# Optimization experiments

Hardware: AMD Instinct MI355X
Metric: run time of the kernel (lower is better)

Reference implementation:

```python
import jax, jax.numpy as jnp
import numpy as np

N_RAYS = 8192
N_SAMPLES = 128
HIDDEN = 128
SH_DIM = 16
RAY_EXT_FACTOR = 10.0


def rsh_cart_3(d):
    # Real spherical harmonics up to degree 3, Cartesian form (16 coeffs).
    x, y, z = d[..., 0], d[..., 1], d[..., 2]
    x2, y2, z2 = x * x, y * y, z * z
    xy, yz, xz = x * y, y * z, x * z
    return jnp.stack([
        0.282094791773878 * jnp.ones_like(x),
        -0.48860251190292 * y,
        0.48860251190292 * z,
        -0.48860251190292 * x,
        1.0925484305920792 * xy,
        -1.0925484305920792 * yz,
        0.94617469575756 * z2 - 0.31539156525252,
        -1.0925484305920792 * xz,
        0.5462742152960396 * (x2 - y2),
        0.5900435899266435 * y * (-3.0 * x2 + y2),
        2.8906114426405538 * xy * z,
        0.4570457994644658 * y * (1.0 - 5.0 * z2),
        0.3731763325901154 * z * (5.0 * z2 - 3.0),
        0.4570457994644658 * x * (1.0 - 5.0 * z2),
        1.445305721320277 * z * (x2 - y2),
        0.5900435899266435 * x * (-x2 + 3.0 * y2),
    ], axis=-1)


def setup_inputs() -> dict:
    key = jax.random.key(0)
    ks = jax.random.split(key, 11)
    o = jax.random.normal(ks[0], (N_RAYS, 3), dtype=jnp.float32)
    origins = 2.5 * o / jnp.linalg.norm(o, axis=-1, keepdims=True)
    # aim roughly at the unit AABB so most rays are active
    dirs = -origins + 0.2 * jax.random.normal(ks[1], (N_RAYS, 3), dtype=jnp.float32)
    u = jax.random.uniform(ks[2], (N_RAYS, N_SAMPLES), dtype=jnp.float32)
    s1 = 1.0 / np.sqrt(3.0)
    s2 = 1.0 / np.sqrt(HIDDEN)
    s3 = 1.0 / np.sqrt(HIDDEN + SH_DIM)
    return {
        'origins': origins,
        'dirs': dirs,
        'u': u,
        'W1': s1 * jax.random.normal(ks[3], (3, HIDDEN), dtype=jnp.float32),
        'b1': jnp.zeros((HIDDEN,), jnp.float32),
        'W2': s2 * jax.random.normal(ks[4], (HIDDEN, HIDDEN), dtype=jnp.float32),
        'b2': jnp.zeros((HIDDEN,), jnp.float32),
        'Wd': s2 * jax.random.normal(ks[5], (HIDDEN, 1), dtype=jnp.float32),
        'bd': jnp.zeros((1,), jnp.float32),
        'Wc': s3 * jax.random.normal(ks[6], (HIDDEN + SH_DIM, 3), dtype=jnp.float32),
        'bc': jnp.zeros((3,), jnp.float32),
    }


def reference(origins, dirs, u, W1, b1, W2, b2, Wd, bd, Wc, bc):
    B, T = u.shape
    # ---- AABB ([-1,1]^3) slab intersection -> tnear/tfar, active mask ----
    inv_d = 1.0 / dirs
    t1 = (-1.0 - origins) * inv_d
    t2 = (1.0 - origins) * inv_d
    tnear = jnp.maximum(jnp.max(jnp.minimum(t1, t2), axis=-1), 0.0)  # (B,)
    tfar = jnp.min(jnp.maximum(t1, t2), axis=-1)                      # (B,)
    active = tfar > tnear                                             # (B,)
    tfar_c = jnp.maximum(tfar, tnear + 1e-3)
    # ---- stratified ray step sampling ----
    frac = (jnp.arange(T, dtype=u.dtype) + u) / T                     # (B,T)
    ts = tnear[:, None] + (tfar_c - tnear)[:, None] * frac            # (B,T)
    xyz = origins[:, None, :] + dirs[:, None, :] * ts[..., None]      # (B,T,3)
    # aabb is [-1,1]^3 so ndc == xyz; spatial filter = bounds test
    xyz_ndc = xyz
    mask = jnp.all(jnp.abs(xyz_ndc) <= 1.0, axis=-1) & active[:, None]  # (B,T)
    dnorm = jnp.linalg.norm(dirs, axis=-1)                            # (B,)
    ynm = rsh_cart_3(dirs / dnorm[:, None])                           # (B,16)
    # ---- radiance field MLP over all sample points ----
    x = xyz_ndc.reshape(B * T, 3)
    h = jax.nn.relu(x @ W1 + b1)
    h = jax.nn.relu(h @ W2 + b2)
    sigma = jax.nn.softplus(h @ Wd + bd).reshape(B, T)
    cond = jnp.broadcast_to(ynm[:, None, :], (B, T, SH_DIM)).reshape(B * T, SH_DIM)
    color = jax.nn.sigmoid(jnp.concatenate([h, cond], axis=-1) @ Wc + bc).reshape(B, T, 3)
    # zero out points rejected by the spatial filter (torch writes only masked)
    sigma = sigma * mask
    color = color * mask[..., None]
    # ---- transmittance integration (integrate_timesteps) ----
    tfinal = tfar_c * RAY_EXT_FACTOR
    deltas = jnp.diff(ts, axis=-1, append=tfinal[:, None])            # (B,T)
    sd = sigma * deltas * dnorm[:, None]
    csum = jnp.cumsum(sd, axis=-1)
    # weights_i = T_i * alpha_i = exp(-csum_{i-1}) - exp(-csum_i)
    weights = jnp.exp(sd - csum) - jnp.exp(-csum)                     # (B,T)
    color_out = jnp.einsum('bt,btc->bc', weights, color)              # (B,3)
    alpha_out = jnp.sum(weights, axis=-1, keepdims=True)              # (B,1)
    rgba = jnp.concatenate([color_out, alpha_out], axis=-1)           # (B,4)
    return jnp.where(active[:, None], rgba, 0.0)
```

## Files before the change

kernel.cpp:

```cpp
#include <hip/hip_runtime.h>
#include <math.h>

#define NRAYS 8192
#define T 128
#define H 128
#define SHD 16

using short8 = __attribute__((ext_vector_type(8))) short;
using f32x4  = __attribute__((ext_vector_type(4))) float;

__device__ __forceinline__ float softplus_f(float x) {
  return fmaxf(x, 0.f) + log1pf(expf(-fabsf(x)));
}

__device__ __forceinline__ unsigned f2bf(float f) {
  unsigned u = __float_as_uint(f);
  return (u + 0x7fffu + ((u >> 16) & 1u)) >> 16;
}

__device__ __forceinline__ unsigned pkbf(float a, float b) {
  const unsigned ua = __float_as_uint(a) + 0x8000u;
  const unsigned ub = __float_as_uint(b) + 0x8000u;
  return __builtin_amdgcn_perm(ub, ua, 0x07060302u);
}

__global__ void preprocess(const float* __restrict__ W2, const float* __restrict__ Wd,
                           const float* __restrict__ Wc,
                           unsigned short* __restrict__ w2t,
                           unsigned short* __restrict__ woutf) {
  const int t = blockIdx.x * 256 + threadIdx.x;
  if (t < 16384) {
    const int n = t >> 7, p = t & 127;
    const int o = (p >> 3) ^ (n & 7);
    const int k = o * 8 + (p & 7);
    w2t[t] = (unsigned short)f2bf(W2[k * 128 + n]);
  }
  if (t < 2048) {
    const int kk = t >> 9, L = (t >> 3) & 63, j = t & 7;
    const int c = L & 15, g = L >> 4;
    const int k = kk * 32 + g * 8 + j;
    float v = 0.f;
    if (c == 0) v = Wd[k];
    else if (c < 4) v = Wc[k * 3 + (c - 1)];
    woutf[t] = (unsigned short)f2bf(v);
  }
}

__global__ __launch_bounds__(256, 3) void nerf_render(
    const float* __restrict__ origins, const float* __restrict__ dirs,
    const float* __restrict__ u, const float* __restrict__ W1,
    const float* __restrict__ b1, const float* __restrict__ b2,
    const float* __restrict__ bd, const float* __restrict__ Wc,
    const float* __restrict__ bc, const unsigned short* __restrict__ w2t,
    const unsigned short* __restrict__ woutf, float* __restrict__ out)
{
  const int ray = blockIdx.x;
  const int tid = threadIdx.x;
  const int L = tid & 63;
  const int w = tid >> 6;
  const int g = L >> 4;
  const int c = L & 15;

  __shared__ __align__(16) short Bs[16384];
  __shared__ __align__(16) short As2[4 * 640];
  __shared__ __align__(16) float2 bsl[H];
  __shared__ float ts_s[T];
  __shared__ float mask_s[T];
  __shared__ __align__(16) float4 SredP[T];
  __shared__ float rayp[8];
  __shared__ float wred[2][4];
  __shared__ float wtot[2];

  {
    const float4* src = (const float4*)w2t;
    float4* dst = (float4*)Bs;
    #pragma unroll
    for (int i = 0; i < 8; ++i) dst[tid + i * 256] = src[tid + i * 256];
  }

  if (tid < T) {
    const int tl = tid;
    const float ox = origins[ray*3+0], oy = origins[ray*3+1], oz = origins[ray*3+2];
    const float dx = dirs[ray*3+0],  dy = dirs[ray*3+1],  dz = dirs[ray*3+2];
    const float ix = 1.f/dx, iy = 1.f/dy, iz = 1.f/dz;
    const float t1x = (-1.f-ox)*ix, t2x = (1.f-ox)*ix;
    const float t1y = (-1.f-oy)*iy, t2y = (1.f-oy)*iy;
    const float t1z = (-1.f-oz)*iz, t2z = (1.f-oz)*iz;
    float tnear = fmaxf(fmaxf(fminf(t1x,t2x), fminf(t1y,t2y)), fminf(t1z,t2z));
    tnear = fmaxf(tnear, 0.f);
    const float tfar = fminf(fminf(fmaxf(t1x,t2x), fmaxf(t1y,t2y)), fmaxf(t1z,t2z));
    const bool  active = tfar > tnear;
    const float tfar_c = fmaxf(tfar, tnear + 1e-3f);
    const float ut = u[ray*T + tl];
    const float frac = ((float)tl + ut) * (1.f/(float)T);
    const float tt = tnear + (tfar_c - tnear) * frac;
    const float px = fmaf(dx, tt, ox);
    const float py = fmaf(dy, tt, oy);
    const float pz = fmaf(dz, tt, oz);
    ts_s[tl] = tt;
    const bool m = (fabsf(px) <= 1.f) && (fabsf(py) <= 1.f) && (fabsf(pz) <= 1.f) && active;
    mask_s[tl] = m ? 1.f : 0.f;
    const float w0 = W1[tl], w1v = W1[H + tl], w2v = W1[2*H + tl];
    bsl[tl] = make_float2(
        fmaf(ox, w0, fmaf(oy, w1v, fmaf(oz, w2v, b1[tl]))),
        fmaf(dx, w0, fmaf(dy, w1v, dz * w2v)));
    if (tl == 0) {
      rayp[0] = tfar_c;
      rayp[1] = sqrtf(dx*dx + dy*dy + dz*dz);
      rayp[2] = active ? 1.f : 0.f;
    }
  } else if (tid == 128) {
    const float dx = dirs[ray*3+0], dy = dirs[ray*3+1], dz = dirs[ray*3+2];
    const float dnorm = sqrtf(dx*dx + dy*dy + dz*dz);
    const float nx = dx/dnorm, ny = dy/dnorm, nz = dz/dnorm;
    const float x2 = nx*nx, y2 = ny*ny, z2 = nz*nz;
    const float xy = nx*ny, yz = ny*nz, xz = nx*nz;
    float ynm[16];
    ynm[0]  = 0.282094791773878f;
    ynm[1]  = -0.48860251190292f*ny;
    ynm[2]  = 0.48860251190292f*nz;
    ynm[3]  = -0.48860251190292f*nx;
    ynm[4]  = 1.0925484305920792f*xy;
    ynm[5]  = -1.0925484305920792f*yz;
    ynm[6]  = 0.94617469575756f*z2 - 0.31539156525252f;
    ynm[7]  = -1.0925484305920792f*xz;
    ynm[8]  = 0.5462742152960396f*(x2-y2);
    ynm[9]  = 0.5900435899266435f*ny*(-3.f*x2+y2);
    ynm[10] = 2.8906114426405538f*xy*nz;
    ynm[11] = 0.4570457994644658f*ny*(1.f-5.f*z2);
    ynm[12] = 0.3731763325901154f*nz*(5.f*z2-3.f);
    ynm[13] = 0.4570457994644658f*nx*(1.f-5.f*z2);
    ynm[14] = 1.445305721320277f*nz*(x2-y2);
    ynm[15] = 0.5900435899266435f*nx*(-x2+3.f*y2);
    float cp0 = bc[0], cp1 = bc[1], cp2 = bc[2];
    #pragma unroll
    for (int s = 0; s < SHD; ++s) {
      cp0 = fmaf(ynm[s], Wc[(H+s)*3+0], cp0);
      cp1 = fmaf(ynm[s], Wc[(H+s)*3+1], cp1);
      cp2 = fmaf(ynm[s], Wc[(H+s)*3+2], cp2);
    }
    rayp[3] = cp0; rayp[4] = cp1; rayp[5] = cp2;
  }

  short8 wa[4];
  #pragma unroll
  for (int kk = 0; kk < 4; ++kk)
    wa[kk] = *(const short8*)&woutf[(kk*64 + L)*8];

  f32x4 acc[2][8];
  #pragma unroll
  for (int mt = 0; mt < 8; ++mt) {
    const float4 bv = *(const float4*)&b2[mt*16 + g*4];
    #pragma unroll
    for (int tm = 0; tm < 2; ++tm) {
      acc[tm][mt][0] = bv.x; acc[tm][mt][1] = bv.y;
      acc[tm][mt][2] = bv.z; acc[tm][mt][3] = bv.w;
    }
  }
  __syncthreads();

  const float t0 = ts_s[32*w + c];
  const float t1 = ts_s[32*w + 16 + c];

  #pragma unroll
  for (int ks = 0; ks < 4; ++ks) {
    const int kb = ks*32 + g*8;
    float ha[8], hb_[8];
    #pragma unroll
    for (int j = 0; j < 8; ++j) {
      const float2 p = bsl[kb + j];
      ha[j]  = fmaxf(fmaf(t0, p.y, p.x), 0.f);
      hb_[j] = fmaxf(fmaf(t1, p.y, p.x), 0.f);
    }
    union U { uint4 u; short8 s; } A0, A1;
    A0.u = make_uint4(pkbf(ha[0],ha[1]),  pkbf(ha[2],ha[3]),  pkbf(ha[4],ha[5]),  pkbf(ha[6],ha[7]));
    A1.u = make_uint4(pkbf(hb_[0],hb_[1]),pkbf(hb_[2],hb_[3]),pkbf(hb_[4],hb_[5]),pkbf(hb_[6],hb_[7]));
    const int swb = ((ks*4 + g) ^ (c & 7)) * 8;
    #pragma unroll
    for (int mt = 0; mt < 8; ++mt) {
      const short8 wf = *(const short8*)&Bs[(mt*16 + c)*128 + swb];
      acc[0][mt] = __builtin_amdgcn_mfma_f32_16x16x32_bf16(wf, A0.s, acc[0][mt], 0, 0, 0);
      acc[1][mt] = __builtin_amdgcn_mfma_f32_16x16x32_bf16(wf, A1.s, acc[1][mt], 0, 0, 0);
    }
  }

  short* As2w = As2 + w * 640;
  #pragma unroll
  for (int tm = 0; tm < 2; ++tm) {
    f32x4 oacc;
    oacc[0] = 0.f; oacc[1] = 0.f; oacc[2] = 0.f; oacc[3] = 0.f;
    #pragma unroll
    for (int kk = 0; kk < 4; ++kk) {
      #pragma unroll
      for (int i = 0; i < 2; ++i) {
        const f32x4 a = acc[tm][kk*2 + i];
        const float h0 = fmaxf(a[0], 0.f);
        const float h1 = fmaxf(a[1], 0.f);
        const float h2 = fmaxf(a[2], 0.f);
        const float h3 = fmaxf(a[3], 0.f);
        *(uint2*)&As2w[c*40 + i*16 + g*4] = make_uint2(pkbf(h0, h1), pkbf(h2, h3));
      }
      const short8 hbf = *(const short8*)&As2w[c*40 + g*8];
      oacc = __builtin_amdgcn_mfma_f32_16x16x32_bf16(wa[kk], hbf, oacc, 0, 0, 0);
    }
    if (g == 0)
      SredP[32*w + 16*tm + c] = make_float4(oacc[0], oacc[1], oacc[2], oacc[3]);
  }
  __syncthreads();

  float sd = 0.f, cc0 = 0.f, cc1 = 0.f, cc2 = 0.f;
  if (tid < T) {
    const float4 sv = SredP[tid];
    const float mk = mask_s[tid];
    const float sigma = softplus_f(sv.x + bd[0]) * mk;
    const float cp0 = sv.y + rayp[3];
    const float cp1 = sv.z + rayp[4];
    const float cp2 = sv.w + rayp[5];
    cc0 = mk / (1.f + expf(-cp0));
    cc1 = mk / (1.f + expf(-cp1));
    cc2 = mk / (1.f + expf(-cp2));
    const float tt = ts_s[tid];
    const float tnext = (tid < T-1) ? ts_s[tid + 1] : rayp[0] * 10.f;
    sd = sigma * (tnext - tt) * rayp[1];
  }

  float val = sd;
  #pragma unroll
  for (int off = 1; off < 64; off <<= 1) {
    const float tmp = __shfl_up(val, off);
    if (L >= off) val += tmp;
  }
  if (tid < T && L == 63) wtot[w] = val;
  __syncthreads();
  const float csum = val + ((w == 1) ? wtot[0] : 0.f);

  float wgt = 0.f, wcx = 0.f, wcy = 0.f, wcz = 0.f;
  if (tid < T) {
    wgt = expf(sd - csum) - expf(-csum);
    wcx = wgt * cc0; wcy = wgt * cc1; wcz = wgt * cc2;
  }
  #pragma unroll
  for (int mm = 32; mm >= 1; mm >>= 1) {
    wgt += __shfl_xor(wgt, mm);
    wcx += __shfl_xor(wcx, mm);
    wcy += __shfl_xor(wcy, mm);
    wcz += __shfl_xor(wcz, mm);
  }
  if (tid < T && L == 0) {
    wred[w][0] = wgt; wred[w][1] = wcx; wred[w][2] = wcy; wred[w][3] = wcz;
  }
  __syncthreads();
  if (tid == 0) {
    const float aw = wred[0][0] + wred[1][0];
    const float o0 = wred[0][1] + wred[1][1];
    const float o1 = wred[0][2] + wred[1][2];
    const float o2 = wred[0][3] + wred[1][3];
    const bool act = rayp[2] != 0.f;
    out[ray*4+0] = act ? o0 : 0.f;
    out[ray*4+1] = act ? o1 : 0.f;
    out[ray*4+2] = act ? o2 : 0.f;
    out[ray*4+3] = act ? aw : 0.f;
  }
}

extern "C" void kernel_launch(void* const* d_in, const int* in_sizes, int n_in,
                              void* d_out, int out_size, void* d_ws, size_t ws_size,
                              hipStream_t stream) {
  const float* origins = (const float*)d_in[0];
  const float* dirs    = (const float*)d_in[1];
  const float* u       = (const float*)d_in[2];
  const float* W1      = (const float*)d_in[3];
  const float* b1      = (const float*)d_in[4];
  const float* W2      = (const float*)d_in[5];
  const float* b2      = (const float*)d_in[6];
  const float* Wd      = (const float*)d_in[7];
  const float* bd      = (const float*)d_in[8];
  const float* Wc      = (const float*)d_in[9];
  const float* bc      = (const float*)d_in[10];

  unsigned short* w2t   = (unsigned short*)d_ws;
  unsigned short* woutf = (unsigned short*)((char*)d_ws + 32768);

  preprocess<<<64, 256, 0, stream>>>(W2, Wd, Wc, w2t, woutf);
  nerf_render<<<NRAYS, 256, 0, stream>>>(origins, dirs, u, W1, b1, b2, bd, Wc, bc,
                                         w2t, woutf, (float*)d_out);
}
```

Baseline: 146.6 us.

## Raise occupancy, reuse weight LDS for reductions, use packed FP32 and fast transcendentals

Launch bounds go from 3 to 4 blocks per CU. LDS use drops because SredP now reuses the Bs weight buffer after an extra barrier. The layer-1 base/slope arrays are split so they can be read with vector loads, and the FMA/max/bf16 packing is done on 2-wide float vectors so the compiler can emit packed FP32 instructions. The wout fragment load moves after the main MFMA loop to shorten register live ranges. expf/log1pf/division are replaced with exp2/log2/rcp approximations, which costs some accuracy and adds one block-wide sync.

```diff
diff --git a/kernel.cpp b/kernel.cpp
--- a/kernel.cpp
+++ b/kernel.cpp
@@ -8,9 +8,17 @@
 
 using short8 = __attribute__((ext_vector_type(8))) short;
 using f32x4  = __attribute__((ext_vector_type(4))) float;
-
+using f32x2  = __attribute__((ext_vector_type(2))) float;
+using u32x2  = __attribute__((ext_vector_type(2))) unsigned;
+
+__device__ __forceinline__ float fexp(float x) {
+  return exp2f(x * 1.44269504088896341f);
+}
 __device__ __forceinline__ float softplus_f(float x) {
-  return fmaxf(x, 0.f) + log1pf(expf(-fabsf(x)));
+  return fmaxf(x, 0.f) + 0.693147180559945309f * log2f(1.f + fexp(-fabsf(x)));
+}
+__device__ __forceinline__ float sigmoid_f(float x) {
+  return __builtin_amdgcn_rcpf(1.f + fexp(-x));
 }
 
 __device__ __forceinline__ unsigned f2bf(float f) {
@@ -18,10 +26,9 @@
   return (u + 0x7fffu + ((u >> 16) & 1u)) >> 16;
 }
 
-__device__ __forceinline__ unsigned pkbf(float a, float b) {
-  const unsigned ua = __float_as_uint(a) + 0x8000u;
-  const unsigned ub = __float_as_uint(b) + 0x8000u;
-  return __builtin_amdgcn_perm(ub, ua, 0x07060302u);
+__device__ __forceinline__ unsigned pk2(f32x2 h) {
+  const u32x2 u = __builtin_bit_cast(u32x2, h) + (u32x2){0x8000u, 0x8000u};
+  return __builtin_amdgcn_perm(u[1], u[0], 0x07060302u);
 }
 
 __global__ void preprocess(const float* __restrict__ W2, const float* __restrict__ Wd,
@@ -46,7 +53,7 @@
   }
 }
 
-__global__ __launch_bounds__(256, 3) void nerf_render(
+__global__ __launch_bounds__(256, 4) void nerf_render(
     const float* __restrict__ origins, const float* __restrict__ dirs,
     const float* __restrict__ u, const float* __restrict__ W1,
     const float* __restrict__ b1, const float* __restrict__ b2,
@@ -63,10 +70,10 @@
 
   __shared__ __align__(16) short Bs[16384];
   __shared__ __align__(16) short As2[4 * 640];
-  __shared__ __align__(16) float2 bsl[H];
+  __shared__ __align__(16) float baseA[H];
+  __shared__ __align__(16) float slopeA[H];
   __shared__ float ts_s[T];
   __shared__ float mask_s[T];
-  __shared__ __align__(16) float4 SredP[T];
   __shared__ float rayp[8];
   __shared__ float wred[2][4];
   __shared__ float wtot[2];
@@ -101,9 +108,8 @@
     const bool m = (fabsf(px) <= 1.f) && (fabsf(py) <= 1.f) && (fabsf(pz) <= 1.f) && active;
     mask_s[tl] = m ? 1.f : 0.f;
     const float w0 = W1[tl], w1v = W1[H + tl], w2v = W1[2*H + tl];
-    bsl[tl] = make_float2(
-        fmaf(ox, w0, fmaf(oy, w1v, fmaf(oz, w2v, b1[tl]))),
-        fmaf(dx, w0, fmaf(dy, w1v, dz * w2v)));
+    baseA[tl]  = fmaf(ox, w0, fmaf(oy, w1v, fmaf(oz, w2v, b1[tl])));
+    slopeA[tl] = fmaf(dx, w0, fmaf(dy, w1v, dz * w2v));
     if (tl == 0) {
       rayp[0] = tfar_c;
       rayp[1] = sqrtf(dx*dx + dy*dy + dz*dz);
@@ -142,11 +148,6 @@
     rayp[3] = cp0; rayp[4] = cp1; rayp[5] = cp2;
   }
 
-  short8 wa[4];
-  #pragma unroll
-  for (int kk = 0; kk < 4; ++kk)
-    wa[kk] = *(const short8*)&woutf[(kk*64 + L)*8];
-
   f32x4 acc[2][8];
   #pragma unroll
   for (int mt = 0; mt < 8; ++mt) {
@@ -161,20 +162,31 @@
 
   const float t0 = ts_s[32*w + c];
   const float t1 = ts_s[32*w + 16 + c];
+  const f32x2 tz0 = {t0, t0}, tz1 = {t1, t1};
+  const f32x2 zero2 = {0.f, 0.f};
 
   #pragma unroll
   for (int ks = 0; ks < 4; ++ks) {
     const int kb = ks*32 + g*8;
-    float ha[8], hb_[8];
-    #pragma unroll
-    for (int j = 0; j < 8; ++j) {
-      const float2 p = bsl[kb + j];
-      ha[j]  = fmaxf(fmaf(t0, p.y, p.x), 0.f);
-      hb_[j] = fmaxf(fmaf(t1, p.y, p.x), 0.f);
-    }
+    const f32x4 bq0 = *(const f32x4*)&baseA[kb];
+    const f32x4 bq1 = *(const f32x4*)&baseA[kb+4];
+    const f32x4 sq0 = *(const f32x4*)&slopeA[kb];
+    const f32x4 sq1 = *(const f32x4*)&slopeA[kb+4];
+    const f32x2 b01 = {bq0[0], bq0[1]}, b23 = {bq0[2], bq0[3]};
+    const f32x2 b45 = {bq1[0], bq1[1]}, b67 = {bq1[2], bq1[3]};
+    const f32x2 s01 = {sq0[0], sq0[1]}, s23 = {sq0[2], sq0[3]};
+    const f32x2 s45 = {sq1[0], sq1[1]}, s67 = {sq1[2], sq1[3]};
+    const f32x2 a01 = __builtin_elementwise_max(__builtin_elementwise_fma(tz0, s01, b01), zero2);
+    const f32x2 a23 = __builtin_elementwise_max(__builtin_elementwise_fma(tz0, s23, b23), zero2);
+    const f32x2 a45 = __builtin_elementwise_max(__builtin_elementwise_fma(tz0, s45, b45), zero2);
+    const f32x2 a67 = __builtin_elementwise_max(__builtin_elementwise_fma(tz0, s67, b67), zero2);
+    const f32x2 e01 = __builtin_elementwise_max(__builtin_elementwise_fma(tz1, s01, b01), zero2);
+    const f32x2 e23 = __builtin_elementwise_max(__builtin_elementwise_fma(tz1, s23, b23), zero2);
+    const f32x2 e45 = __builtin_elementwise_max(__builtin_elementwise_fma(tz1, s45, b45), zero2);
+    const f32x2 e67 = __builtin_elementwise_max(__builtin_elementwise_fma(tz1, s67, b67), zero2);
     union U { uint4 u; short8 s; } A0, A1;
-    A0.u = make_uint4(pkbf(ha[0],ha[1]),  pkbf(ha[2],ha[3]),  pkbf(ha[4],ha[5]),  pkbf(ha[6],ha[7]));
-    A1.u = make_uint4(pkbf(hb_[0],hb_[1]),pkbf(hb_[2],hb_[3]),pkbf(hb_[4],hb_[5]),pkbf(hb_[6],hb_[7]));
+    A0.u = make_uint4(pk2(a01), pk2(a23), pk2(a45), pk2(a67));
+    A1.u = make_uint4(pk2(e01), pk2(e23), pk2(e45), pk2(e67));
     const int swb = ((ks*4 + g) ^ (c & 7)) * 8;
     #pragma unroll
     for (int mt = 0; mt < 8; ++mt) {
@@ -183,8 +195,15 @@
       acc[1][mt] = __builtin_amdgcn_mfma_f32_16x16x32_bf16(wf, A1.s, acc[1][mt], 0, 0, 0);
     }
   }
+  __syncthreads();
+  float4* SredP = (float4*)Bs;
 
   short* As2w = As2 + w * 640;
+  short8 wa[4];
+  #pragma unroll
+  for (int kk = 0; kk < 4; ++kk)
+    wa[kk] = *(const short8*)&woutf[(kk*64 + L)*8];
+
   #pragma unroll
   for (int tm = 0; tm < 2; ++tm) {
     f32x4 oacc;
@@ -194,11 +213,9 @@
       #pragma unroll
       for (int i = 0; i < 2; ++i) {
         const f32x4 a = acc[tm][kk*2 + i];
-        const float h0 = fmaxf(a[0], 0.f);
-        const float h1 = fmaxf(a[1], 0.f);
-        const float h2 = fmaxf(a[2], 0.f);
-        const float h3 = fmaxf(a[3], 0.f);
-        *(uint2*)&As2w[c*40 + i*16 + g*4] = make_uint2(pkbf(h0, h1), pkbf(h2, h3));
+        const f32x2 h01 = __builtin_elementwise_max((f32x2){a[0], a[1]}, zero2);
+        const f32x2 h23 = __builtin_elementwise_max((f32x2){a[2], a[3]}, zero2);
+        *(uint2*)&As2w[c*40 + i*16 + g*4] = make_uint2(pk2(h01), pk2(h23));
       }
       const short8 hbf = *(const short8*)&As2w[c*40 + g*8];
       oacc = __builtin_amdgcn_mfma_f32_16x16x32_bf16(wa[kk], hbf, oacc, 0, 0, 0);
@@ -213,12 +230,9 @@
     const float4 sv = SredP[tid];
     const float mk = mask_s[tid];
     const float sigma = softplus_f(sv.x + bd[0]) * mk;
-    const float cp0 = sv.y + rayp[3];
-    const float cp1 = sv.z + rayp[4];
-    const float cp2 = sv.w + rayp[5];
-    cc0 = mk / (1.f + expf(-cp0));
-    cc1 = mk / (1.f + expf(-cp1));
-    cc2 = mk / (1.f + expf(-cp2));
+    cc0 = mk * sigmoid_f(sv.y + rayp[3]);
+    cc1 = mk * sigmoid_f(sv.z + rayp[4]);
+    cc2 = mk * sigmoid_f(sv.w + rayp[5]);
     const float tt = ts_s[tid];
     const float tnext = (tid < T-1) ? ts_s[tid + 1] : rayp[0] * 10.f;
     sd = sigma * (tnext - tt) * rayp[1];
@@ -236,7 +250,7 @@
 
   float wgt = 0.f, wcx = 0.f, wcy = 0.f, wcz = 0.f;
   if (tid < T) {
-    wgt = expf(sd - csum) - expf(-csum);
+    wgt = fexp(sd - csum) - fexp(-csum);
     wcx = wgt * cc0; wcy = wgt * cc1; wcz = wgt * cc2;
   }
   #pragma unroll
```

New measurement: 135.0 us. 8.0% less time.
